# Kernel tuning notes

Hardware: AMD Instinct MI355X
Metric: run time of the kernel (lower is better)

Reference implementation:

```python
import jax, jax.numpy as jnp
import numpy as np

N = 100000   # nodes
E = 1000000  # edges
F_IN = 64    # input node features
EMB = 32     # init_emb
C = 32       # hidden/out channels per head
H = 4        # heads
HC = H * C   # 128
NEG_SLOPE = 0.2


def setup_inputs() -> dict:
    key = jax.random.key(0)
    ks = jax.random.split(key, 40)
    g = lambda k, shape: jax.random.normal(k, shape, jnp.float32) * 0.05
    inp = {
        "x": jax.random.normal(ks[0], (N, F_IN), jnp.float32),
        "edge_index": jax.random.randint(ks[1], (2, E), 0, N, jnp.int32),
        "W0": g(ks[2], (F_IN, EMB)),
    }
    i = 3
    for p, din in (("f", EMB), ("m", HC), ("l", HC)):
        inp[p + "_Wl"] = g(ks[i], (din, HC)); i += 1
        inp[p + "_bl"] = g(ks[i], (HC,));     i += 1
        inp[p + "_Wr"] = g(ks[i], (din, HC)); i += 1
        inp[p + "_br"] = g(ks[i], (HC,));     i += 1
        inp[p + "_att"] = g(ks[i], (H, C));   i += 1
        inp[p + "_cb"] = g(ks[i], (HC,));     i += 1
        inp[p + "_Ws"] = g(ks[i], (din, HC)); i += 1
        inp[p + "_bs"] = g(ks[i], (HC,));     i += 1
    return inp


def _gatv2(x, src, dst, Wl, bl, Wr, br, att, cb):
    # GATv2Conv, bipartite weights, concat heads, add_self_loops=False
    xl = (x @ Wl + bl).reshape(-1, H, C)  # source transform [N,H,C]
    xr = (x @ Wr + br).reshape(-1, H, C)  # target transform [N,H,C]
    e = xl[src] + xr[dst]                 # [E,H,C]
    s = jnp.where(e > 0, e, NEG_SLOPE * e)
    score = jnp.einsum('ehc,hc->eh', s, att)  # [E,H]
    mmax = jax.ops.segment_max(score, dst, num_segments=N)
    ex = jnp.exp(score - mmax[dst])
    den = jax.ops.segment_sum(ex, dst, num_segments=N)
    alpha = ex / den[dst]                 # segment softmax over in-edges
    out = jax.ops.segment_sum(xl[src] * alpha[:, :, None], dst, num_segments=N)
    return out.reshape(-1, HC) + cb


def reference(x, edge_index,
              W0,
              f_Wl, f_bl, f_Wr, f_br, f_att, f_cb, f_Ws, f_bs,
              m_Wl, m_bl, m_Wr, m_br, m_att, m_cb, m_Ws, m_bs,
              l_Wl, l_bl, l_Wr, l_br, l_att, l_cb, l_Ws, l_bs):
    src, dst = edge_index[0], edge_index[1]
    h = jax.nn.relu(x @ W0)
    h = jax.nn.relu(_gatv2(h, src, dst, f_Wl, f_bl, f_Wr, f_br, f_att, f_cb) + h @ f_Ws + f_bs)
    for _ in range(3):  # conv_mid / lin_mid weights are SHARED across the 3 iterations
        h = jax.nn.relu(_gatv2(h, src, dst, m_Wl, m_bl, m_Wr, m_br, m_att, m_cb) + h @ m_Ws + m_bs)
    h = _gatv2(h, src, dst, l_Wl, l_bl, l_Wr, l_br, l_att, l_cb) + h @ l_Ws + l_bs
    h = h / jnp.linalg.norm(h, axis=-1, keepdims=True)
    return h
```

## Files before the change

kernel.cpp:

```cpp
#include <hip/hip_runtime.h>
#include <hip/hip_bf16.h>
#include <math.h>

#define N_NODES 100000
#define N_EDGES 1000000
#define NEG_SLOPE 0.2f
#define NBUCK 98
#define BSHIFT 10
#define SLAB 12288
#define BINA_EDGES 4096

typedef short v8s __attribute__((ext_vector_type(8)));
typedef float v4f __attribute__((ext_vector_type(4)));

__device__ inline unsigned pack_bf16(float a, float b) {
    unsigned ua = __float_as_uint(a);
    unsigned ub = __float_as_uint(b);
    ua = (ua + 0x7FFFu + ((ua >> 16) & 1u)) >> 16;
    ub = (ub + 0x7FFFu + ((ub >> 16) & 1u)) >> 16;
    return ua | (ub << 16);
}
__device__ inline unsigned short bf16_rn(float x) {
    unsigned u = __float_as_uint(x);
    u = (u + 0x7FFFu + ((u >> 16) & 1u)) >> 16;
    return (unsigned short)u;
}
__device__ inline void unpack8(uint4 u, float* f) {
    f[0] = __uint_as_float(u.x << 16); f[1] = __uint_as_float(u.x & 0xFFFF0000u);
    f[2] = __uint_as_float(u.y << 16); f[3] = __uint_as_float(u.y & 0xFFFF0000u);
    f[4] = __uint_as_float(u.z << 16); f[5] = __uint_as_float(u.z & 0xFFFF0000u);
    f[6] = __uint_as_float(u.w << 16); f[7] = __uint_as_float(u.w & 0xFFFF0000u);
}


__global__ __launch_bounds__(256) void binA_kernel(
    const int* __restrict__ src, const int* __restrict__ dst,
    int* __restrict__ gcursor, int* __restrict__ tmp) {
    __shared__ int bstart[NBUCK];
    __shared__ int addrbase[NBUCK];
    __shared__ int bcur[NBUCK];
    __shared__ int s[256];
    __shared__ int staged_val[BINA_EDGES];
    __shared__ int staged_addr[BINA_EDGES];
    const int tid = threadIdx.x;
    const int base = blockIdx.x * BINA_EDGES;
    const int ecount = min(BINA_EDGES, N_EDGES - base);

    if (tid < NBUCK) bcur[tid] = 0;
    __syncthreads();
    for (int j = tid; j < ecount; j += 256) {
        int d = dst[base + j];
        atomicAdd(&bcur[d >> BSHIFT], 1);
    }
    __syncthreads();
    int own = (tid < NBUCK) ? bcur[tid] : 0;
    s[tid] = own;
    __syncthreads();
    for (int off = 1; off < 256; off <<= 1) {
        int u = (tid >= off) ? s[tid - off] : 0;
        __syncthreads();
        s[tid] += u;
        __syncthreads();
    }
    if (tid < NBUCK) {
        int excl = s[tid] - own;
        bstart[tid] = excl;
        int resv = atomicAdd(&gcursor[tid], own);
        addrbase[tid] = resv - excl;
    }
    __syncthreads();
    if (tid < NBUCK) bcur[tid] = bstart[tid];
    __syncthreads();
    for (int j = tid; j < ecount; j += 256) {
        int d = dst[base + j];
        int sr = src[base + j];
        int bk = d >> BSHIFT;
        int lpos = atomicAdd(&bcur[bk], 1);
        staged_val[lpos] = ((d & ((1 << BSHIFT) - 1)) << 17) | sr;
        staged_addr[lpos] = addrbase[bk] + lpos;
    }
    __syncthreads();
    for (int j = tid; j < ecount; j += 256)
        tmp[staged_addr[j]] = staged_val[j];
}

__global__ void bucket_scan(const int* __restrict__ gcursor, int* __restrict__ bbase,
                            int* __restrict__ row_ptr) {
    __shared__ int s[128];
    int t = threadIdx.x;
    int v = (t < NBUCK) ? (gcursor[t] - t * SLAB) : 0;
    s[t] = v;
    __syncthreads();
    for (int off = 1; off < 128; off <<= 1) {
        int u = (t >= off) ? s[t - off] : 0;
        __syncthreads();
        s[t] += u;
        __syncthreads();
    }
    if (t < NBUCK) bbase[t] = s[t] - v;
    if (t == 0) row_ptr[N_NODES] = N_EDGES;
}

__global__ __launch_bounds__(256) void binB_kernel(
    const int* __restrict__ tmp, const int* __restrict__ gcursor,
    const int* __restrict__ bbase, int* __restrict__ row_ptr,
    int* __restrict__ srcs) {
    __shared__ int hist[1024];
    __shared__ int tsum[256];
    const int b = blockIdx.x;
    const int tid = threadIdx.x;
    const int base = b * SLAB;
    const int cnt = gcursor[b] - base;
    const int node0 = b << BSHIFT;
    const int nodes_in = min(1024, N_NODES - node0);
    const int gb = bbase[b];

    for (int i = tid; i < 1024; i += 256) hist[i] = 0;
    __syncthreads();
    for (int i = tid; i < cnt; i += 256)
        atomicAdd(&hist[tmp[base + i] >> 17], 1);
    __syncthreads();
    int v[4], local = 0;
#pragma unroll
    for (int j = 0; j < 4; ++j) {
        v[j] = hist[tid * 4 + j];
        local += v[j];
    }
    tsum[tid] = local;
    __syncthreads();
    for (int off = 1; off < 256; off <<= 1) {
        int u = (tid >= off) ? tsum[tid - off] : 0;
        __syncthreads();
        tsum[tid] += u;
        __syncthreads();
    }
    int run = tsum[tid] - local;
#pragma unroll
    for (int j = 0; j < 4; ++j) {
        hist[tid * 4 + j] = run;
        run += v[j];
    }
    __syncthreads();
    for (int i = tid; i < nodes_in; i += 256)
        row_ptr[node0 + i] = gb + hist[i];
    __syncthreads();
    for (int i = tid; i < cnt; i += 256) {
        int e = tmp[base + i];
        int pos = atomicAdd(&hist[e >> 17], 1);
        srcs[gb + pos] = e & 0x1FFFF;
    }
}

__device__ inline void conv_one(int idx, int K, const float* __restrict__ Wl,
                                const float* __restrict__ Wr, const float* __restrict__ Ws,
                                unsigned short* __restrict__ wt) {
    int n = idx / K;
    int k = idx - n * K;
    int sec = n >> 7;
    int nn = n & 127;
    const float* W = (sec == 0) ? Wl : (sec == 1) ? Wr : Ws;
    wt[idx] = bf16_rn(W[k * 128 + nn]);
}

__global__ void convert_all(
    const float* __restrict__ fWl, const float* __restrict__ fWr, const float* __restrict__ fWs,
    const float* __restrict__ mWl, const float* __restrict__ mWr, const float* __restrict__ mWs,
    const float* __restrict__ lWl, const float* __restrict__ lWr, const float* __restrict__ lWs,
    unsigned short* __restrict__ wt_f, unsigned short* __restrict__ wt_m,
    unsigned short* __restrict__ wt_l, int* __restrict__ gcursor) {
    int t = blockIdx.x * blockDim.x + threadIdx.x;
    if (t < NBUCK) gcursor[t] = t * SLAB;
    if (t < 384 * 32) {
        conv_one(t, 32, fWl, fWr, fWs, wt_f);
    } else if (t < 384 * 32 + 384 * 128) {
        conv_one(t - 384 * 32, 128, mWl, mWr, mWs, wt_m);
    } else if (t < 384 * 32 + 2 * 384 * 128) {
        conv_one(t - 384 * 32 - 384 * 128, 128, lWl, lWr, lWs, wt_l);
    }
}

__global__ void h0_kernel(const float* __restrict__ x, const float* __restrict__ W0,
                          unsigned short* __restrict__ h) {
    int tid = blockIdx.x * blockDim.x + threadIdx.x;
    int col = tid & 31;
    int row = tid >> 5;
    if (row >= N_NODES) return;
    const float* xr = x + row * 64;
    float acc = 0.f;
#pragma unroll
    for (int k = 0; k < 64; ++k) acc = fmaf(xr[k], W0[k * 32 + col], acc);
    h[row * 32 + col] = bf16_rn(fmaxf(acc, 0.f));
}

template <int K>
__global__ __launch_bounds__(64) void mm3_mfma(
    const unsigned short* __restrict__ A, const unsigned short* __restrict__ Wt,
    const float* __restrict__ bl, const float* __restrict__ br, const float* __restrict__ bs,
    const float* __restrict__ cb,
    unsigned short* __restrict__ xl_bf, unsigned short* __restrict__ xr_bf,
    unsigned short* __restrict__ sk_bf) {
    const int lane = threadIdx.x & 63;
    const int q = lane >> 4;
    const int li = lane & 15;
    const int r0 = blockIdx.x * 32;
    constexpr int KS = K / 32;

    v8s a[2][KS];
#pragma unroll
    for (int mi = 0; mi < 2; ++mi) {
        int row = r0 + mi * 16 + li;
        row = row < N_NODES ? row : N_NODES - 1;
#pragma unroll
        for (int ks = 0; ks < KS; ++ks)
            a[mi][ks] = *(const v8s*)&A[(size_t)row * K + ks * 32 + q * 8];
    }

    for (int t = 0; t < 6; ++t) {
        const int sec = t >> 1;
        const int c0 = (t & 1) * 64;
        v4f acc[2][4];
#pragma unroll
        for (int mi = 0; mi < 2; ++mi)
#pragma unroll
            for (int ni = 0; ni < 4; ++ni) acc[mi][ni] = (v4f)(0.f);

#pragma unroll
        for (int ks = 0; ks < KS; ++ks) {
            v8s b[4];
#pragma unroll
            for (int ni = 0; ni < 4; ++ni) {
                int col = sec * 128 + c0 + ni * 16 + li;
                b[ni] = *(const v8s*)&Wt[(size_t)col * K + ks * 32 + q * 8];
            }
#pragma unroll
            for (int mi = 0; mi < 2; ++mi)
#pragma unroll
                for (int ni = 0; ni < 4; ++ni)
                    acc[mi][ni] = __builtin_amdgcn_mfma_f32_16x16x32_bf16(b[ni], a[mi][ks], acc[mi][ni], 0, 0, 0);
        }

        unsigned short* dstp = (sec == 0) ? xl_bf : (sec == 1) ? xr_bf : sk_bf;
#pragma unroll
        for (int ni = 0; ni < 4; ++ni) {
            int cbase = c0 + ni * 16 + q * 4;
            float4 b4;
            if (sec == 0) b4 = *(const float4*)&bl[cbase];
            else if (sec == 1) b4 = *(const float4*)&br[cbase];
            else {
                float4 t1 = *(const float4*)&bs[cbase];
                float4 t2 = *(const float4*)&cb[cbase];
                b4 = make_float4(t1.x + t2.x, t1.y + t2.y, t1.z + t2.z, t1.w + t2.w);
            }
#pragma unroll
            for (int mi = 0; mi < 2; ++mi) {
                int row = r0 + mi * 16 + li;
                if (row >= N_NODES) continue;
                v4f v = acc[mi][ni];
                uint2 pk;
                pk.x = pack_bf16(v[0] + b4.x, v[1] + b4.y);
                pk.y = pack_bf16(v[2] + b4.z, v[3] + b4.w);
                *(uint2*)&dstp[(size_t)row * 128 + cbase] = pk;
            }
        }
    }
}

#define GATHER4(S) (*(const uint4*)((const char*)xlb4 + (((unsigned)(S)) << 8) + ((unsigned)li << 4)))

#define AGG_BODY(XC, SVC, CB)                                               \
    {                                                                       \
        float xf[8];                                                        \
        unpack8(XC, xf);                                                    \
        bool vld = (CB) + g < end;                                          \
        if ((CB) + 12 < end) XC = GATHER4(SVC);                             \
        if ((CB) + 24 < end) {                                              \
            int ii = (CB) + 24 + g;                                         \
            SVC = srcs[ii < end ? ii : em1];                                \
        }                                                                   \
        float p1 = 0.f, p2 = 0.f;                                           \
        _Pragma("unroll") for (int i = 0; i < 8; ++i) {                     \
            float e_ = xf[i] + xr_f[i];                                     \
            p1 = fmaf(e_, at_f[i], p1);                                     \
            p2 = fmaf(fabsf(e_), at_f[i], p2);                              \
        }                                                                   \
        float p = fmaf(0.6f, p1, 0.4f * p2);                                \
        p += __shfl_xor(p, 1);                                              \
        p += __shfl_xor(p, 2);                                              \
        float w = vld ? __expf(p) : 0.f;                                    \
        lsum += w;                                                          \
        _Pragma("unroll") for (int i = 0; i < 8; ++i)                       \
            acc[i] = fmaf(xf[i], w, acc[i]);                                \
    }

__global__ __launch_bounds__(256, 7) void agg_kernel(
    const uint4* __restrict__ xlb4, const uint4* __restrict__ xrb4,
    const uint4* __restrict__ skb4, const int* __restrict__ row_ptr,
    const int* __restrict__ srcs, const float* __restrict__ att,
    uint4* __restrict__ out_bf, float* __restrict__ out_f,
    int write_bf, int do_relu, int do_norm) {
    int n = (blockIdx.x * blockDim.x + threadIdx.x) >> 6;
    if (n >= N_NODES) return;
    int lane = threadIdx.x & 63;
    int g = lane >> 4, li = lane & 15;

    const int beg = __builtin_amdgcn_readfirstlane(row_ptr[n]);
    const int end = __builtin_amdgcn_readfirstlane(row_ptr[n + 1]);

    uint4 xru = xrb4[(size_t)n * 16 + li];
    uint4 sku = skb4[(size_t)n * 16 + li];

    float at_f[8];
    *(float4*)&at_f[0] = *(const float4*)&att[li * 8];
    *(float4*)&at_f[4] = *(const float4*)&att[li * 8 + 4];
    float xr_f[8];
    unpack8(xru, xr_f);

    float acc[8];
#pragma unroll
    for (int i = 0; i < 8; ++i) acc[i] = 0.f;
    float lsum = 0.f;

    if (beg < end) {
        const int em1 = end - 1;
#define SRC_AT(Q) ({ int _ii = beg + (Q) * 4 + g; srcs[_ii < end ? _ii : em1]; })
        int sv0 = SRC_AT(0), sv1 = SRC_AT(1), sv2 = SRC_AT(2);
        uint4 x0 = {}, x1 = {}, x2 = {};
        x0 = GATHER4(sv0);
        if (beg + 4 < end) x1 = GATHER4(sv1);
        if (beg + 8 < end) x2 = GATHER4(sv2);
        sv0 = SRC_AT(3);
        sv1 = SRC_AT(4);
        sv2 = SRC_AT(5);
#undef SRC_AT

        for (int cb = beg; cb < end; cb += 12) {
            AGG_BODY(x0, sv0, cb)
            if (cb + 4 < end) AGG_BODY(x1, sv1, cb + 4)
            if (cb + 8 < end) AGG_BODY(x2, sv2, cb + 8)
        }
    }

#pragma unroll
    for (int i = 0; i < 8; ++i) {
        acc[i] += __shfl_xor(acc[i], 16);
        acc[i] += __shfl_xor(acc[i], 32);
    }
    lsum += __shfl_xor(lsum, 16);
    lsum += __shfl_xor(lsum, 32);

    float inv = (lsum > 0.f) ? 1.f / lsum : 0.f;
    float sk_f[8];
    unpack8(sku, sk_f);
    float o[8];
#pragma unroll
    for (int i = 0; i < 8; ++i) o[i] = fmaf(acc[i], inv, sk_f[i]);
    if (do_relu) {
#pragma unroll
        for (int i = 0; i < 8; ++i) o[i] = fmaxf(o[i], 0.f);
    }
    if (do_norm) {
        float ss = 0.f;
#pragma unroll
        for (int i = 0; i < 8; ++i) ss = fmaf(o[i], o[i], ss);
        ss += __shfl_xor(ss, 1);
        ss += __shfl_xor(ss, 2);
        ss += __shfl_xor(ss, 4);
        ss += __shfl_xor(ss, 8);
        float r = 1.0f / sqrtf(ss);
#pragma unroll
        for (int i = 0; i < 8; ++i) o[i] *= r;
    }
    if (g == 0) {
        if (write_bf) {
            uint4 pk;
            pk.x = pack_bf16(o[0], o[1]);
            pk.y = pack_bf16(o[2], o[3]);
            pk.z = pack_bf16(o[4], o[5]);
            pk.w = pack_bf16(o[6], o[7]);
            out_bf[(size_t)n * 16 + li] = pk;
        } else {
            *(float4*)&out_f[(size_t)n * 128 + li * 8] = make_float4(o[0], o[1], o[2], o[3]);
            *(float4*)&out_f[(size_t)n * 128 + li * 8 + 4] = make_float4(o[4], o[5], o[6], o[7]);
        }
    }
}

extern "C" void kernel_launch(void* const* d_in, const int* in_sizes, int n_in,
                              void* d_out, int out_size, void* d_ws, size_t ws_size,
                              hipStream_t stream) {
    const float* x = (const float*)d_in[0];
    const int* ei = (const int*)d_in[1];
    const int* src = ei;
    const int* dst = ei + N_EDGES;
    const float* W0 = (const float*)d_in[2];

    const float* f_p[8];
    const float* m_p[8];
    const float* l_p[8];
    for (int i = 0; i < 8; ++i) f_p[i] = (const float*)d_in[3 + i];
    for (int i = 0; i < 8; ++i) m_p[i] = (const float*)d_in[11 + i];
    for (int i = 0; i < 8; ++i) l_p[i] = (const float*)d_in[19 + i];

    char* ws = (char*)d_ws;
    unsigned short* xl_bf = (unsigned short*)ws; ws += (size_t)N_NODES * 128 * 2;
    unsigned short* xr_bf = (unsigned short*)ws; ws += (size_t)N_NODES * 128 * 2;
    unsigned short* sk_bf = (unsigned short*)ws; ws += (size_t)N_NODES * 128 * 2;
    unsigned short* h_bf = (unsigned short*)ws;  ws += (size_t)N_NODES * 128 * 2;
    int* row_ptr = (int*)ws;       ws += (size_t)(N_NODES + 1) * 4;
    int* srcs = (int*)ws;          ws += (size_t)N_EDGES * 4;
    int* tmp = (int*)ws;           ws += (size_t)NBUCK * SLAB * 4;
    int* gcursor = (int*)ws;       ws += (size_t)NBUCK * 4;
    int* bbase = (int*)ws;         ws += (size_t)NBUCK * 4;
    unsigned short* wt_f = (unsigned short*)ws; ws += (size_t)384 * 32 * 2;
    unsigned short* wt_m = (unsigned short*)ws; ws += (size_t)384 * 128 * 2;
    unsigned short* wt_l = (unsigned short*)ws; ws += (size_t)384 * 128 * 2;

    const int conv_total = 384 * 32 + 2 * 384 * 128;
    convert_all<<<(conv_total + 255) / 256, 256, 0, stream>>>(
        f_p[0], f_p[2], f_p[6], m_p[0], m_p[2], m_p[6], l_p[0], l_p[2], l_p[6],
        wt_f, wt_m, wt_l, gcursor);
    binA_kernel<<<(N_EDGES + BINA_EDGES - 1) / BINA_EDGES, 256, 0, stream>>>(src, dst, gcursor, tmp);
    bucket_scan<<<1, 128, 0, stream>>>(gcursor, bbase, row_ptr);
    binB_kernel<<<NBUCK, 256, 0, stream>>>(tmp, gcursor, bbase, row_ptr, srcs);

    h0_kernel<<<(N_NODES * 32) / 256, 256, 0, stream>>>(x, W0, h_bf);

    const int gmm = (N_NODES + 31) / 32;
    const int gagg = (N_NODES * 64) / 256;
    float* out = (float*)d_out;

    mm3_mfma<32><<<gmm, 64, 0, stream>>>(h_bf, wt_f, f_p[1], f_p[3], f_p[7], f_p[5],
                                         xl_bf, xr_bf, sk_bf);
    agg_kernel<<<gagg, 256, 0, stream>>>((uint4*)xl_bf, (uint4*)xr_bf, (uint4*)sk_bf,
                                         row_ptr, srcs, f_p[4],
                                         (uint4*)h_bf, nullptr, 1, 1, 0);

    for (int it = 0; it < 3; ++it) {
        mm3_mfma<128><<<gmm, 64, 0, stream>>>(h_bf, wt_m, m_p[1], m_p[3], m_p[7], m_p[5],
                                              xl_bf, xr_bf, sk_bf);
        agg_kernel<<<gagg, 256, 0, stream>>>((uint4*)xl_bf, (uint4*)xr_bf, (uint4*)sk_bf,
                                             row_ptr, srcs, m_p[4],
                                             (uint4*)h_bf, nullptr, 1, 1, 0);
    }

    mm3_mfma<128><<<gmm, 64, 0, stream>>>(h_bf, wt_l, l_p[1], l_p[3], l_p[7], l_p[5],
                                          xl_bf, xr_bf, sk_bf);
    agg_kernel<<<gagg, 256, 0, stream>>>((uint4*)xl_bf, (uint4*)xr_bf, (uint4*)sk_bf,
                                         row_ptr, srcs, l_p[4],
                                         nullptr, out, 0, 0, 1);
}
```

Measured before the change: 731.8 us.

## Widen MFMA row tile, stage outputs through LDS, spread agg stores

```diff
diff --git a/kernel.cpp b/kernel.cpp
--- a/kernel.cpp
+++ b/kernel.cpp
@@ -199,28 +199,32 @@
     const float* __restrict__ cb,
     unsigned short* __restrict__ xl_bf, unsigned short* __restrict__ xr_bf,
     unsigned short* __restrict__ sk_bf) {
+    __shared__ uint4 tile4[64 * 10];
     const int lane = threadIdx.x & 63;
     const int q = lane >> 4;
     const int li = lane & 15;
-    const int r0 = blockIdx.x * 32;
+    const int r0 = blockIdx.x * 64;
     constexpr int KS = K / 32;
 
-    v8s a[2][KS];
-#pragma unroll
-    for (int mi = 0; mi < 2; ++mi) {
+    v8s a[4][KS];
+#pragma unroll
+    for (int mi = 0; mi < 4; ++mi) {
         int row = r0 + mi * 16 + li;
         row = row < N_NODES ? row : N_NODES - 1;
 #pragma unroll
         for (int ks = 0; ks < KS; ++ks)
             a[mi][ks] = *(const v8s*)&A[(size_t)row * K + ks * 32 + q * 8];
     }
+
+    const int frow = lane >> 3;
+    const int fchunk = lane & 7;
 
     for (int t = 0; t < 6; ++t) {
         const int sec = t >> 1;
         const int c0 = (t & 1) * 64;
-        v4f acc[2][4];
-#pragma unroll
-        for (int mi = 0; mi < 2; ++mi)
+        v4f acc[4][4];
+#pragma unroll
+        for (int mi = 0; mi < 4; ++mi)
 #pragma unroll
             for (int ni = 0; ni < 4; ++ni) acc[mi][ni] = (v4f)(0.f);
 
@@ -233,7 +237,7 @@
                 b[ni] = *(const v8s*)&Wt[(size_t)col * K + ks * 32 + q * 8];
             }
 #pragma unroll
-            for (int mi = 0; mi < 2; ++mi)
+            for (int mi = 0; mi < 4; ++mi)
 #pragma unroll
                 for (int ni = 0; ni < 4; ++ni)
                     acc[mi][ni] = __builtin_amdgcn_mfma_f32_16x16x32_bf16(b[ni], a[mi][ks], acc[mi][ni], 0, 0, 0);
@@ -252,14 +256,22 @@
                 b4 = make_float4(t1.x + t2.x, t1.y + t2.y, t1.z + t2.z, t1.w + t2.w);
             }
 #pragma unroll
-            for (int mi = 0; mi < 2; ++mi) {
-                int row = r0 + mi * 16 + li;
-                if (row >= N_NODES) continue;
+            for (int mi = 0; mi < 4; ++mi) {
                 v4f v = acc[mi][ni];
                 uint2 pk;
                 pk.x = pack_bf16(v[0] + b4.x, v[1] + b4.y);
                 pk.y = pack_bf16(v[2] + b4.z, v[3] + b4.w);
-                *(uint2*)&dstp[(size_t)row * 128 + cbase] = pk;
+                int lrow = mi * 16 + li;
+                *(uint2*)((char*)tile4 + lrow * 160 + ni * 32 + q * 8) = pk;
+            }
+        }
+#pragma unroll
+        for (int j = 0; j < 8; ++j) {
+            int lrow = j * 8 + frow;
+            int grow = r0 + lrow;
+            if (grow < N_NODES) {
+                uint4 v = *(const uint4*)((const char*)tile4 + lrow * 160 + fchunk * 16);
+                *(uint4*)((char*)dstp + (size_t)grow * 256 + c0 * 2 + fchunk * 16) = v;
             }
         }
     }
@@ -296,7 +308,7 @@
     const uint4* __restrict__ xlb4, const uint4* __restrict__ xrb4,
     const uint4* __restrict__ skb4, const int* __restrict__ row_ptr,
     const int* __restrict__ srcs, const float* __restrict__ att,
-    uint4* __restrict__ out_bf, float* __restrict__ out_f,
+    unsigned* __restrict__ out_bf, float* __restrict__ out_f,
     int write_bf, int do_relu, int do_norm) {
     int n = (blockIdx.x * blockDim.x + threadIdx.x) >> 6;
     if (n >= N_NODES) return;
@@ -324,10 +336,9 @@
         const int em1 = end - 1;
 #define SRC_AT(Q) ({ int _ii = beg + (Q) * 4 + g; srcs[_ii < end ? _ii : em1]; })
         int sv0 = SRC_AT(0), sv1 = SRC_AT(1), sv2 = SRC_AT(2);
-        uint4 x0 = {}, x1 = {}, x2 = {};
-        x0 = GATHER4(sv0);
-        if (beg + 4 < end) x1 = GATHER4(sv1);
-        if (beg + 8 < end) x2 = GATHER4(sv2);
+        uint4 x0 = GATHER4(sv0);
+        uint4 x1 = GATHER4(sv1);
+        uint4 x2 = GATHER4(sv2);
         sv0 = SRC_AT(3);
         sv1 = SRC_AT(4);
         sv2 = SRC_AT(5);
@@ -370,18 +381,14 @@
 #pragma unroll
         for (int i = 0; i < 8; ++i) o[i] *= r;
     }
-    if (g == 0) {
-        if (write_bf) {
-            uint4 pk;
-            pk.x = pack_bf16(o[0], o[1]);
-            pk.y = pack_bf16(o[2], o[3]);
-            pk.z = pack_bf16(o[4], o[5]);
-            pk.w = pack_bf16(o[6], o[7]);
-            out_bf[(size_t)n * 16 + li] = pk;
-        } else {
-            *(float4*)&out_f[(size_t)n * 128 + li * 8] = make_float4(o[0], o[1], o[2], o[3]);
-            *(float4*)&out_f[(size_t)n * 128 + li * 8 + 4] = make_float4(o[4], o[5], o[6], o[7]);
-        }
+
+    float oa = (g == 0) ? o[0] : (g == 1) ? o[2] : (g == 2) ? o[4] : o[6];
+    float ob = (g == 0) ? o[1] : (g == 1) ? o[3] : (g == 2) ? o[5] : o[7];
+    if (write_bf) {
+        *(unsigned*)((char*)out_bf + (size_t)n * 256 + li * 16 + g * 4) = pack_bf16(oa, ob);
+    } else {
+        float2 v2 = make_float2(oa, ob);
+        *(float2*)((char*)out_f + (size_t)n * 512 + li * 32 + g * 8) = v2;
     }
 }
 
@@ -425,7 +432,7 @@
 
     h0_kernel<<<(N_NODES * 32) / 256, 256, 0, stream>>>(x, W0, h_bf);
 
-    const int gmm = (N_NODES + 31) / 32;
+    const int gmm = (N_NODES + 63) / 64;
     const int gagg = (N_NODES * 64) / 256;
     float* out = (float*)d_out;
 
@@ -433,14 +440,14 @@
                                          xl_bf, xr_bf, sk_bf);
     agg_kernel<<<gagg, 256, 0, stream>>>((uint4*)xl_bf, (uint4*)xr_bf, (uint4*)sk_bf,
                                          row_ptr, srcs, f_p[4],
-                                         (uint4*)h_bf, nullptr, 1, 1, 0);
+                                         (unsigned*)h_bf, nullptr, 1, 1, 0);
 
     for (int it = 0; it < 3; ++it) {
         mm3_mfma<128><<<gmm, 64, 0, stream>>>(h_bf, wt_m, m_p[1], m_p[3], m_p[7], m_p[5],
                                               xl_bf, xr_bf, sk_bf);
         agg_kernel<<<gagg, 256, 0, stream>>>((uint4*)xl_bf, (uint4*)xr_bf, (uint4*)sk_bf,
                                              row_ptr, srcs, m_p[4],
-                                             (uint4*)h_bf, nullptr, 1, 1, 0);
+                                             (unsigned*)h_bf, nullptr, 1, 1, 0);
     }
 
     mm3_mfma<128><<<gmm, 64, 0, stream>>>(h_bf, wt_l, l_p[1], l_p[3], l_p[7], l_p[5],
```

Result: faster. 632.0 us (-13.6%).
